# Performance work log

Hardware: AMD Instinct MI355X
Metric: run time of the kernel (lower is better)

The kernel has to match this reference:

```python
import math
import jax, jax.numpy as jnp
import numpy as np

D = 256      # embedding_dim (= internal_dim, downsample_rate 1)
H = 8        # num_heads
HD = D // H  # head_dim = 32
NTC = 16     # num_text_classes
NIMG = 4096  # image tokens (64x64)
N = NIMG + NTC
B = 2
NKE = 64     # num_k_exclude_rope


def _rope(x, freqs):
    # x: (b, h, n, c); freqs: (n, c//2, 2) = (cos, sin) of complex rotary factors
    b, h, n, c = x.shape
    xp = x.reshape(b, h, n, c // 2, 2)
    cos, sin = freqs[..., 0], freqs[..., 1]
    xr, xi = xp[..., 0], xp[..., 1]
    out_r = xr * cos - xi * sin
    out_i = xr * sin + xi * cos
    return jnp.stack([out_r, out_i], axis=-1).reshape(b, h, n, c)


def _sep_heads(x):
    b, n, c = x.shape
    return x.reshape(b, n, H, c // H).transpose(0, 2, 1, 3)  # (b,h,n,hd)


def setup_inputs() -> dict:
    key = jax.random.key(0)
    ks = jax.random.split(key, 14)
    s = 0.02
    # rotary factors: unit-norm cos/sin pairs
    ang_img = jax.random.uniform(ks[3], (NIMG, HD // 2)) * (2.0 * np.pi)
    ang_txt = jax.random.uniform(ks[4], (NTC, HD // 2)) * (2.0 * np.pi)
    return {
        "q": jax.random.normal(ks[0], (B, N, D), dtype=jnp.float32),
        "k": jax.random.normal(ks[1], (B, N, D), dtype=jnp.float32),
        "v": jax.random.normal(ks[2], (B, N, D), dtype=jnp.float32),
        "freqs_cis_img": jnp.stack([jnp.cos(ang_img), jnp.sin(ang_img)], axis=-1),
        "freqs_cis_txt": jnp.stack([jnp.cos(ang_txt), jnp.sin(ang_txt)], axis=-1),
        "Wq": jax.random.normal(ks[5], (D, D), dtype=jnp.float32) * s,
        "bq": jnp.zeros((D,), dtype=jnp.float32),
        "Wk": jax.random.normal(ks[6], (D, D), dtype=jnp.float32) * s,
        "bk": jnp.zeros((D,), dtype=jnp.float32),
        "Wv": jax.random.normal(ks[7], (D, D), dtype=jnp.float32) * s,
        "bv": jnp.zeros((D,), dtype=jnp.float32),
        "Wo": jax.random.normal(ks[8], (D, D), dtype=jnp.float32) * s,
        "bo": jnp.zeros((D,), dtype=jnp.float32),
        "num_k_exclude_rope": NKE,
    }


def reference(q, k, v, freqs_cis_img, freqs_cis_txt,
              Wq, bq, Wk, bk, Wv, bv, Wo, bo, num_k_exclude_rope):
    q = q @ Wq.T + bq
    k = k @ Wk.T + bk
    v = v @ Wv.T + bv
    q = _sep_heads(q)  # (b,h,n,hd)
    k = _sep_heads(k)
    v = _sep_heads(v)

    # split tokens into image / text regions, apply RoPE separately
    q_img, q_txt = q[:, :, :-NTC, :], q[:, :, -NTC:, :]
    k_img, k_txt = k[:, :, :-NTC, :], k[:, :, -NTC:, :]
    q_img = _rope(q_img, freqs_cis_img)
    k_img = _rope(k_img, freqs_cis_img)
    q_txt = _rope(q_txt, freqs_cis_txt)
    k_txt = _rope(k_txt, freqs_cis_txt)
    q = jnp.concatenate([q_img, q_txt], axis=-2)
    k = jnp.concatenate([k_img, k_txt], axis=-2)

    scale = 1.0 / math.sqrt(HD)
    nke = num_k_exclude_rope
    if nke > 0:
        k_td, k_mem = k[:, :, :-nke, :], k[:, :, -nke:, :]
        v_td, v_mem = v[:, :, :-nke, :], v[:, :, -nke:, :]
        attn = jax.nn.softmax(jnp.einsum('bhqd,bhkd->bhqk', q, k_td) * scale, axis=-1)
        out = jnp.einsum('bhqk,bhkd->bhqd', attn, v_td)
        attn_m = jax.nn.softmax(jnp.einsum('bhqd,bhkd->bhqk', q, k_mem) * scale, axis=-1)
        out = out + jnp.einsum('bhqk,bhkd->bhqd', attn_m, v_mem)
    else:
        attn = jax.nn.softmax(jnp.einsum('bhqd,bhkd->bhqk', q, k) * scale, axis=-1)
        out = jnp.einsum('bhqk,bhkd->bhqd', attn, v)

    b, h, n, hd = out.shape
    out = out.transpose(0, 2, 1, 3).reshape(b, n, h * hd)
    return out @ Wo.T + bo
```

## Files before the change

### kernel.cpp

```cpp
#include <hip/hip_runtime.h>
#include <hip/hip_bf16.h>

#define BN    4112
#define NKR   4160
#define BNP   4160
#define BB    2
#define HH    8
#define NIMG_ 4096
#define NMAIN 4048
#define MROWS 8224
#define QSCALE 0.25505402f

typedef __attribute__((ext_vector_type(8))) short short8;
typedef __attribute__((ext_vector_type(4))) float f32x4;
typedef __attribute__((ext_vector_type(16))) float f32x16;

__device__ __forceinline__ unsigned short f2bs(float x) { return __bfloat16_as_ushort(__float2bfloat16(x)); }
__device__ __forceinline__ unsigned pkbf(float a, float b) {
    __hip_bfloat162 h = __float22bfloat162_rn(make_float2(a, b));
    unsigned u; __builtin_memcpy(&u, &h, 4); return u;
}
__device__ __forceinline__ float fexp2(float x) {
#if __has_builtin(__builtin_amdgcn_exp2f)
    return __builtin_amdgcn_exp2f(x);
#else
    return exp2f(x);
#endif
}

__global__ __launch_bounds__(256)
void qkv_mfma(const float* __restrict__ Aq, const float* __restrict__ Ak, const float* __restrict__ Av,
              const float* __restrict__ Wq, const float* __restrict__ Wk, const float* __restrict__ Wv,
              const float* __restrict__ bq, const float* __restrict__ bk, const float* __restrict__ bv,
              short* __restrict__ Qr, short* __restrict__ Kr, short* __restrict__ Vt,
              const float* __restrict__ fimg, const float* __restrict__ ftxt)
{
    __shared__ __align__(16) short Ws[2][64][72];
    __shared__ __align__(16) short Ds[2][64][72];

    const int mode = blockIdx.z;
    const float* A    = (mode == 0) ? Aq : (mode == 1) ? Ak : Av;
    const float* W    = (mode == 0) ? Wq : (mode == 1) ? Wk : Wv;
    const float* bias = (mode == 0) ? bq : (mode == 1) ? bk : bv;

    const int t    = threadIdx.x;
    const int wave = t >> 6, lane = t & 63, q16 = lane & 15, quad = lane >> 4;
    const int f0 = blockIdx.x * 64;
    const int m0 = blockIdx.y * 64;
    const int sr = t >> 2, sc = (t & 3) * 16;
    const int arow = m0 + sr;
    const bool aval = arow < MROWS;
    const float* wp = W + (size_t)(f0 + sr) * 256 + sc;
    const float* ap = A + (size_t)(aval ? arow : 0) * 256 + sc;

    f32x4 acc[4] = {{0,0,0,0},{0,0,0,0},{0,0,0,0},{0,0,0,0}};

    uint4 wr0, wr1, dr0, dr1;
    {
        float4 a0 = *(const float4*)(wp),     a1 = *(const float4*)(wp + 4);
        float4 a2 = *(const float4*)(wp + 8), a3 = *(const float4*)(wp + 12);
        wr0 = uint4{pkbf(a0.x,a0.y), pkbf(a0.z,a0.w), pkbf(a1.x,a1.y), pkbf(a1.z,a1.w)};
        wr1 = uint4{pkbf(a2.x,a2.y), pkbf(a2.z,a2.w), pkbf(a3.x,a3.y), pkbf(a3.z,a3.w)};
        a0 = *(const float4*)(ap);     a1 = *(const float4*)(ap + 4);
        a2 = *(const float4*)(ap + 8); a3 = *(const float4*)(ap + 12);
        dr0 = uint4{pkbf(a0.x,a0.y), pkbf(a0.z,a0.w), pkbf(a1.x,a1.y), pkbf(a1.z,a1.w)};
        dr1 = uint4{pkbf(a2.x,a2.y), pkbf(a2.z,a2.w), pkbf(a3.x,a3.y), pkbf(a3.z,a3.w)};
    }
    *(uint4*)&Ws[0][sr][sc] = wr0; *(uint4*)&Ws[0][sr][sc + 8] = wr1;
    *(uint4*)&Ds[0][sr][sc] = dr0; *(uint4*)&Ds[0][sr][sc + 8] = dr1;
    __syncthreads();

    #pragma unroll
    for (int ki = 0; ki < 4; ++ki) {
        const int buf = ki & 1;
        if (ki < 3) {
            const int k1 = (ki + 1) * 64;
            float4 a0 = *(const float4*)(wp + k1),     a1 = *(const float4*)(wp + k1 + 4);
            float4 a2 = *(const float4*)(wp + k1 + 8), a3 = *(const float4*)(wp + k1 + 12);
            wr0 = uint4{pkbf(a0.x,a0.y), pkbf(a0.z,a0.w), pkbf(a1.x,a1.y), pkbf(a1.z,a1.w)};
            wr1 = uint4{pkbf(a2.x,a2.y), pkbf(a2.z,a2.w), pkbf(a3.x,a3.y), pkbf(a3.z,a3.w)};
            a0 = *(const float4*)(ap + k1);     a1 = *(const float4*)(ap + k1 + 4);
            a2 = *(const float4*)(ap + k1 + 8); a3 = *(const float4*)(ap + k1 + 12);
            dr0 = uint4{pkbf(a0.x,a0.y), pkbf(a0.z,a0.w), pkbf(a1.x,a1.y), pkbf(a1.z,a1.w)};
            dr1 = uint4{pkbf(a2.x,a2.y), pkbf(a2.z,a2.w), pkbf(a3.x,a3.y), pkbf(a3.z,a3.w)};
        }
        #pragma unroll
        for (int ks = 0; ks < 2; ++ks) {
            const short8 af = *(const short8*)&Ws[buf][wave * 16 + q16][ks * 32 + quad * 8];
            #pragma unroll
            for (int ct = 0; ct < 4; ++ct) {
                const short8 bf = *(const short8*)&Ds[buf][ct * 16 + q16][ks * 32 + quad * 8];
                acc[ct] = __builtin_amdgcn_mfma_f32_16x16x32_bf16(af, bf, acc[ct], 0, 0, 0);
            }
        }
        if (ki < 3) {
            *(uint4*)&Ws[buf ^ 1][sr][sc] = wr0; *(uint4*)&Ws[buf ^ 1][sr][sc + 8] = wr1;
            *(uint4*)&Ds[buf ^ 1][sr][sc] = dr0; *(uint4*)&Ds[buf ^ 1][sr][sc + 8] = dr1;
            __syncthreads();
        }
    }

    const int fbase = f0 + wave * 16 + quad * 4;
    const float4 bb = *(const float4*)(bias + fbase);
    float vs[4][4];
    #pragma unroll
    for (int ct = 0; ct < 4; ++ct) {
        int n = m0 + ct * 16 + q16;
        float v0 = acc[ct][0] + bb.x, v1 = acc[ct][1] + bb.y;
        float v2 = acc[ct][2] + bb.z, v3 = acc[ct][3] + bb.w;
        int b  = (n >= BN) ? 1 : 0;
        int nb = n - b * BN;
        if (mode < 2) {
            int j0 = (fbase & 31) >> 1;
            const float* fr = (nb < NIMG_) ? (fimg + ((size_t)nb * 16 + j0) * 2)
                                           : (ftxt + ((size_t)(nb - NIMG_) * 16 + j0) * 2);
            float4 cs = *(const float4*)fr;
            float r0 = v0 * cs.x - v1 * cs.y, i0 = v0 * cs.y + v1 * cs.x;
            float r1 = v2 * cs.z - v3 * cs.w, i1 = v2 * cs.w + v3 * cs.z;
            v0 = r0; v1 = i0; v2 = r1; v3 = i1;
        }
        if (mode == 2) {
            vs[ct][0] = v0; vs[ct][1] = v1; vs[ct][2] = v2; vs[ct][3] = v3;
            continue;
        }
        if (n >= MROWS) continue;
        const int h = (fbase >> 5) & 7, hd = fbase & 31;
        if (mode == 0) {
            unsigned short* op = (unsigned short*)Qr + (((size_t)(b * HH + h) * BN + nb) * 32 + hd);
            *(uint2*)op = uint2{pkbf(v0 * QSCALE, v1 * QSCALE), pkbf(v2 * QSCALE, v3 * QSCALE)};
        } else {
            int nk = nb + ((nb >= NMAIN) ? 48 : 0);
            unsigned short* op = (unsigned short*)Kr + (((size_t)(b * HH + h) * NKR + nk) * 32 + hd);
            *(uint2*)op = uint2{pkbf(v0, v1), pkbf(v2, v3)};
        }
    }

    if (mode == 2) {
        short (*Tr)[72] = Ds[0];
        const int fl = wave * 16 + quad * 4;
        #pragma unroll
        for (int ct = 0; ct < 4; ++ct) {
            const int nl = ct * 16 + q16;
            Tr[fl + 0][nl] = (short)f2bs(vs[ct][0]);
            Tr[fl + 1][nl] = (short)f2bs(vs[ct][1]);
            Tr[fl + 2][nl] = (short)f2bs(vs[ct][2]);
            Tr[fl + 3][nl] = (short)f2bs(vs[ct][3]);
        }
        __syncthreads();
        const int h0 = (f0 >> 5) & 7;
        #pragma unroll
        for (int ii = 0; ii < 2; ++ii) {
            const int r  = ii * 32 + (t >> 3);
            const int c8 = (t & 7) * 8;
            const int ng = m0 + c8;
            if (ng < MROWS) {
                uint4 val = *(const uint4*)&Tr[r][c8];
                int b  = (ng >= BN) ? 1 : 0;
                int nb = ng - b * BN;
                int nk = nb + ((nb >= NMAIN) ? 48 : 0);
                int h  = h0 + (r >> 5), hd = r & 31;
                unsigned short* op = (unsigned short*)Vt + ((size_t)(b * HH + h) * 32 + hd) * BNP + nk;
                *(uint4*)op = val;
            }
        }
    }

    if (blockIdx.x == 0 && blockIdx.y < 16 && t < 192) {
        const int bh = blockIdx.y;
        if (mode == 1) {
            short* base = Kr + (size_t)bh * NKR * 32 + (size_t)NMAIN * 32;
            *(uint4*)(base + t * 8) = uint4{0u, 0u, 0u, 0u};
        } else if (mode == 2) {
            short* base = Vt + (size_t)bh * 32 * BNP + (size_t)(t / 6) * BNP + NMAIN + (t % 6) * 8;
            *(uint4*)base = uint4{0u, 0u, 0u, 0u};
        }
    }
}

__global__ __launch_bounds__(256, 4)
void attn_mfma(const short* __restrict__ Qr, const short* __restrict__ Kr,
               const short* __restrict__ Vt, unsigned short* __restrict__ AO)
{
    __shared__ __align__(16) short Ks[2][2][64][40];
    __shared__ __align__(16) short Vs[2][2][32][72];

    const int t    = threadIdx.x;
    const int wave = t >> 6, lane = t & 63, q32 = lane & 31, hi = lane >> 5;
    const int grp  = wave >> 1, w2 = wave & 1;
    const int bh = blockIdx.y;
    const int q  = blockIdx.x * 64 + w2 * 32 + q32;
    const int qc = (q < BN) ? q : (BN - 1);
    const short* qp = Qr + ((size_t)bh * BN + qc) * 32 + hi * 8;
    const short8 qf0 = *(const short8*)(qp);
    const short8 qf1 = *(const short8*)(qp + 16);

    f32x16 oAx = {0,0,0,0,0,0,0,0,0,0,0,0,0,0,0,0};
    f32x16 oAy = {0,0,0,0,0,0,0,0,0,0,0,0,0,0,0,0};
    f32x16 oBx = {0,0,0,0,0,0,0,0,0,0,0,0,0,0,0,0};
    const f32x16 z16 = {0,0,0,0,0,0,0,0,0,0,0,0,0,0,0,0};
    float LA = 0.f, LB = 0.f;

    const int tg = t & 127;
    const int kr = tg >> 2, kc = tg & 3;
    const int vr = tg >> 3, vc = tg & 7;
    const short* kg = Kr + (size_t)bh * NKR * 32 + (size_t)grp * 65536 + (size_t)kr * 32 + kc * 8;
    const short* vg = Vt + (size_t)bh * 32 * BNP + (size_t)vr * BNP + grp * 2048
                         + (vc >> 1) * 16 + (vc & 1) * 4;
    const int ntiles = 32 + grp;

    auto tile = [&](int buf, f32x16& ox, f32x16& oy, float& L) {
        const short8 kf00 = *(const short8*)&Ks[grp][buf][q32][hi * 8];
        const short8 kf01 = *(const short8*)&Ks[grp][buf][q32][16 + hi * 8];
        const short8 kf10 = *(const short8*)&Ks[grp][buf][32 + q32][hi * 8];
        const short8 kf11 = *(const short8*)&Ks[grp][buf][32 + q32][16 + hi * 8];
        f32x16 s0 = __builtin_amdgcn_mfma_f32_32x32x16_bf16(kf00, qf0, z16, 0, 0, 0);
        f32x16 s1 = __builtin_amdgcn_mfma_f32_32x32x16_bf16(kf10, qf0, z16, 0, 0, 0);
        s0 = __builtin_amdgcn_mfma_f32_32x32x16_bf16(kf01, qf1, s0, 0, 0, 0);
        s1 = __builtin_amdgcn_mfma_f32_32x32x16_bf16(kf11, qf1, s1, 0, 0, 0);
        float p0[16], p1[16];
        #pragma unroll
        for (int r = 0; r < 16; ++r) p0[r] = fexp2(s0[r]);
        #pragma unroll
        for (int r = 0; r < 16; ++r) p1[r] = fexp2(s1[r]);
        float l0 = (((p0[0]+p0[1])+(p0[2]+p0[3])) + ((p0[4]+p0[5])+(p0[6]+p0[7])))
                 + (((p0[8]+p0[9])+(p0[10]+p0[11])) + ((p0[12]+p0[13])+(p0[14]+p0[15])));
        float l1 = (((p1[0]+p1[1])+(p1[2]+p1[3])) + ((p1[4]+p1[5])+(p1[6]+p1[7])))
                 + (((p1[8]+p1[9])+(p1[10]+p1[11])) + ((p1[12]+p1[13])+(p1[14]+p1[15])));
        #pragma unroll
        for (int m = 0; m < 2; ++m) {
            uint4 pbu = uint4{pkbf(p0[8*m+0], p0[8*m+1]), pkbf(p0[8*m+2], p0[8*m+3]),
                              pkbf(p0[8*m+4], p0[8*m+5]), pkbf(p0[8*m+6], p0[8*m+7])};
            short8 pb; __builtin_memcpy(&pb, &pbu, 16);
            const short8 vf = *(const short8*)&Vs[grp][buf][q32][m * 16 + hi * 8];
            ox = __builtin_amdgcn_mfma_f32_32x32x16_bf16(vf, pb, ox, 0, 0, 0);
        }
        #pragma unroll
        for (int m = 0; m < 2; ++m) {
            uint4 pbu = uint4{pkbf(p1[8*m+0], p1[8*m+1]), pkbf(p1[8*m+2], p1[8*m+3]),
                              pkbf(p1[8*m+4], p1[8*m+5]), pkbf(p1[8*m+6], p1[8*m+7])};
            short8 pb; __builtin_memcpy(&pb, &pbu, 16);
            const short8 vf = *(const short8*)&Vs[grp][buf][q32][32 + m * 16 + hi * 8];
            oy = __builtin_amdgcn_mfma_f32_32x32x16_bf16(vf, pb, oy, 0, 0, 0);
        }
        L += l0 + l1;
    };

    *(uint4*)&Ks[grp][0][kr][kc * 8]      = *(const uint4*)(kg);
    *(uint4*)&Ks[grp][0][kr + 32][kc * 8] = *(const uint4*)(kg + 1024);
    {
        uint2 a0 = *(const uint2*)(vg),              b0 = *(const uint2*)(vg + 8);
        uint2 a1 = *(const uint2*)(vg + 16 * BNP),   b1 = *(const uint2*)(vg + 16 * BNP + 8);
        *(uint4*)&Vs[grp][0][vr][vc * 8]      = uint4{a0.x, a0.y, b0.x, b0.y};
        *(uint4*)&Vs[grp][0][vr + 16][vc * 8] = uint4{a1.x, a1.y, b1.x, b1.y};
    }
    __syncthreads();

    for (int it = 0; it < 33; ++it) {
        const int buf = it & 1;
        uint4 kreg0, kreg1; uint2 va0, vb0, va1, vb1;
        const bool pre = (it + 1) < ntiles;
        if (pre) {
            const short* kp = kg + (size_t)(it + 1) * 2048;
            kreg0 = *(const uint4*)(kp);
            kreg1 = *(const uint4*)(kp + 1024);
            const short* vp = vg + (it + 1) * 64;
            va0 = *(const uint2*)(vp);            vb0 = *(const uint2*)(vp + 8);
            va1 = *(const uint2*)(vp + 16 * BNP); vb1 = *(const uint2*)(vp + 16 * BNP + 8);
        }
        if (it < ntiles) {
            __builtin_amdgcn_s_setprio(1);
            if (grp == 0)      tile(buf, oAx, oAy, LA);
            else if (it < 32)  tile(buf, oAx, oAy, LA);
            else               tile(buf, oBx, oBx, LB);
            __builtin_amdgcn_s_setprio(0);
        }
        if (pre) {
            *(uint4*)&Ks[grp][buf ^ 1][kr][kc * 8]      = kreg0;
            *(uint4*)&Ks[grp][buf ^ 1][kr + 32][kc * 8] = kreg1;
            *(uint4*)&Vs[grp][buf ^ 1][vr][vc * 8]      = uint4{va0.x, va0.y, vb0.x, vb0.y};
            *(uint4*)&Vs[grp][buf ^ 1][vr + 16][vc * 8] = uint4{va1.x, va1.y, vb1.x, vb1.y};
        }
        __syncthreads();
    }

    f32x16 oA = oAx + oAy;
    f32x16 oB = oBx;

    LA += __shfl_xor(LA, 32);
    LB += __shfl_xor(LB, 32);

    float* ex = (float*)&Ks[0][0][0][0];
    const int slot = (w2 * 64 + lane) * 20;
    if (grp == 0) {
        #pragma unroll
        for (int i = 0; i < 4; ++i)
            *(f32x4*)(ex + slot + 4 * i) = f32x4{oA[4*i], oA[4*i+1], oA[4*i+2], oA[4*i+3]};
        ex[slot + 16] = LA;
    }
    __syncthreads();

    if (grp == 1 && q < BN) {
        float LT = LA + ex[slot + 16] - 48.f;
        const float iA = 1.f / LT, iB = 1.f / LB;
        const int b = bh >> 3, h = bh & 7;
        unsigned short* ap = AO + ((size_t)b * BN + q) * 256 + h * 32;
        #pragma unroll
        for (int k = 0; k < 4; ++k) {
            f32x4 a = *(const f32x4*)(ex + slot + 4 * k);
            float w0 = (oA[4*k+0] + a[0]) * iA + oB[4*k+0] * iB;
            float w1 = (oA[4*k+1] + a[1]) * iA + oB[4*k+1] * iB;
            float w2 = (oA[4*k+2] + a[2]) * iA + oB[4*k+2] * iB;
            float w3 = (oA[4*k+3] + a[3]) * iA + oB[4*k+3] * iB;
            *(uint2*)(ap + 8 * k + 4 * hi) = uint2{pkbf(w0, w1), pkbf(w2, w3)};
        }
    }
}

__global__ __launch_bounds__(256)
void gemm_out(const unsigned short* __restrict__ A, const float* __restrict__ W,
              const float* __restrict__ bias, float* __restrict__ out)
{
    __shared__ __align__(16) short Ws[2][64][72];
    __shared__ __align__(16) short Ds[2][64][72];
    const int t    = threadIdx.x;
    const int wave = t >> 6, lane = t & 63, q16 = lane & 15, quad = lane >> 4;
    const int f0 = blockIdx.x * 64, m0 = blockIdx.y * 64;
    const int sr = t >> 2, sc = (t & 3) * 16;
    const int arow = m0 + sr;
    const bool aval = arow < MROWS;
    const float* wp = W + (size_t)(f0 + sr) * 256 + sc;
    const unsigned short* ap = A + (size_t)(aval ? arow : 0) * 256 + sc;

    f32x4 acc[4] = {{0,0,0,0},{0,0,0,0},{0,0,0,0},{0,0,0,0}};

    uint4 wr0, wr1, dr0, dr1;
    {
        float4 a0 = *(const float4*)(wp),     a1 = *(const float4*)(wp + 4);
        float4 a2 = *(const float4*)(wp + 8), a3 = *(const float4*)(wp + 12);
        wr0 = uint4{pkbf(a0.x,a0.y), pkbf(a0.z,a0.w), pkbf(a1.x,a1.y), pkbf(a1.z,a1.w)};
        wr1 = uint4{pkbf(a2.x,a2.y), pkbf(a2.z,a2.w), pkbf(a3.x,a3.y), pkbf(a3.z,a3.w)};
        dr0 = *(const uint4*)(ap); dr1 = *(const uint4*)(ap + 8);
    }
    *(uint4*)&Ws[0][sr][sc] = wr0; *(uint4*)&Ws[0][sr][sc + 8] = wr1;
    *(uint4*)&Ds[0][sr][sc] = dr0; *(uint4*)&Ds[0][sr][sc + 8] = dr1;
    __syncthreads();

    #pragma unroll
    for (int ki = 0; ki < 4; ++ki) {
        const int buf = ki & 1;
        if (ki < 3) {
            const int k1 = (ki + 1) * 64;
            float4 a0 = *(const float4*)(wp + k1),     a1 = *(const float4*)(wp + k1 + 4);
            float4 a2 = *(const float4*)(wp + k1 + 8), a3 = *(const float4*)(wp + k1 + 12);
            wr0 = uint4{pkbf(a0.x,a0.y), pkbf(a0.z,a0.w), pkbf(a1.x,a1.y), pkbf(a1.z,a1.w)};
            wr1 = uint4{pkbf(a2.x,a2.y), pkbf(a2.z,a2.w), pkbf(a3.x,a3.y), pkbf(a3.z,a3.w)};
            dr0 = *(const uint4*)(ap + k1); dr1 = *(const uint4*)(ap + k1 + 8);
        }
        #pragma unroll
        for (int ks = 0; ks < 2; ++ks) {
            const short8 af = *(const short8*)&Ws[buf][wave * 16 + q16][ks * 32 + quad * 8];
            #pragma unroll
            for (int ct = 0; ct < 4; ++ct) {
                const short8 bf = *(const short8*)&Ds[buf][ct * 16 + q16][ks * 32 + quad * 8];
                acc[ct] = __builtin_amdgcn_mfma_f32_16x16x32_bf16(af, bf, acc[ct], 0, 0, 0);
            }
        }
        if (ki < 3) {
            *(uint4*)&Ws[buf ^ 1][sr][sc] = wr0; *(uint4*)&Ws[buf ^ 1][sr][sc + 8] = wr1;
            *(uint4*)&Ds[buf ^ 1][sr][sc] = dr0; *(uint4*)&Ds[buf ^ 1][sr][sc + 8] = dr1;
            __syncthreads();
        }
    }

    const int fbase = f0 + wave * 16 + quad * 4;
    const float4 bb = *(const float4*)(bias + fbase);
    #pragma unroll
    for (int ct = 0; ct < 4; ++ct) {
        int n = m0 + ct * 16 + q16;
        if (n >= MROWS) continue;
        float* op = out + (size_t)n * 256 + fbase;
        *(float4*)op = float4{acc[ct][0] + bb.x, acc[ct][1] + bb.y,
                              acc[ct][2] + bb.z, acc[ct][3] + bb.w};
    }
}

extern "C" void kernel_launch(void* const* d_in, const int* in_sizes, int n_in,
                              void* d_out, int out_size, void* d_ws, size_t ws_size,
                              hipStream_t stream)
{
    (void)in_sizes; (void)n_in; (void)out_size; (void)ws_size;
    const float* q    = (const float*)d_in[0];
    const float* k    = (const float*)d_in[1];
    const float* v    = (const float*)d_in[2];
    const float* fimg = (const float*)d_in[3];
    const float* ftxt = (const float*)d_in[4];
    const float* Wq   = (const float*)d_in[5];
    const float* bq   = (const float*)d_in[6];
    const float* Wk   = (const float*)d_in[7];
    const float* bk   = (const float*)d_in[8];
    const float* Wv   = (const float*)d_in[9];
    const float* bv   = (const float*)d_in[10];
    const float* Wo   = (const float*)d_in[11];
    const float* bo   = (const float*)d_in[12];

    char* w = (char*)d_ws;
    short*          Qr = (short*)(w);
    short*          Kr = (short*)(w + 4210688);
    short*          Vt = (short*)(w + 8470528);
    unsigned short* AO = (unsigned short*)(w + 12730368);

    qkv_mfma<<<dim3(4, 129, 3), 256, 0, stream>>>(q, k, v, Wq, Wk, Wv, bq, bk, bv,
                                                  Qr, Kr, Vt, fimg, ftxt);
    attn_mfma<<<dim3(65, 16), 256, 0, stream>>>(Qr, Kr, Vt, AO);
    gemm_out<<<dim3(4, 129), 256, 0, stream>>>(AO, Wo, bo, (float*)d_out);
}
```

Before: 202.2 us.

## Prefetch K/V two tiles ahead and remap attention grid for XCD locality

The attention loop now issues global K/V loads two tiles ahead, using two register staging sets, and is unrolled by two so loads overlap more MFMA/exp work. The grid is flattened to 1D with an index remap that round-robins heads across consecutive block IDs, so each head's K/V blocks share an L2/XCD. The extra staging registers may raise register pressure and lower occupancy.

```diff
diff --git a/kernel.cpp b/kernel.cpp
--- a/kernel.cpp
+++ b/kernel.cpp
@@ -187,8 +187,13 @@
     const int t    = threadIdx.x;
     const int wave = t >> 6, lane = t & 63, q32 = lane & 31, hi = lane >> 5;
     const int grp  = wave >> 1, w2 = wave & 1;
-    const int bh = blockIdx.y;
-    const int q  = blockIdx.x * 64 + w2 * 32 + q32;
+
+    const int b_   = blockIdx.x;
+    const int idx  = b_ >> 3;
+    const int bh   = ((b_ & 7) << 1) + (idx >= 65 ? 1 : 0);
+    const int bx   = idx - (idx >= 65 ? 65 : 0);
+
+    const int q  = bx * 64 + w2 * 32 + q32;
     const int qc = (q < BN) ? q : (BN - 1);
     const short* qp = Qr + ((size_t)bh * BN + qc) * 32 + hi * 8;
     const short8 qf0 = *(const short8*)(qp);
@@ -207,6 +212,22 @@
     const short* vg = Vt + (size_t)bh * 32 * BNP + (size_t)vr * BNP + grp * 2048
                          + (vc >> 1) * 16 + (vc & 1) * 4;
     const int ntiles = 32 + grp;
+
+    struct Stage { uint4 k0, k1; uint2 a0, b0, a1, b1; };
+    auto issue = [&](int tix, Stage& s) {
+        const short* kp = kg + (size_t)tix * 2048;
+        s.k0 = *(const uint4*)(kp);
+        s.k1 = *(const uint4*)(kp + 1024);
+        const short* vp = vg + tix * 64;
+        s.a0 = *(const uint2*)(vp);            s.b0 = *(const uint2*)(vp + 8);
+        s.a1 = *(const uint2*)(vp + 16 * BNP); s.b1 = *(const uint2*)(vp + 16 * BNP + 8);
+    };
+    auto commit = [&](int buf, const Stage& s) {
+        *(uint4*)&Ks[grp][buf][kr][kc * 8]      = s.k0;
+        *(uint4*)&Ks[grp][buf][kr + 32][kc * 8] = s.k1;
+        *(uint4*)&Vs[grp][buf][vr][vc * 8]      = uint4{s.a0.x, s.a0.y, s.b0.x, s.b0.y};
+        *(uint4*)&Vs[grp][buf][vr + 16][vc * 8] = uint4{s.a1.x, s.a1.y, s.b1.x, s.b1.y};
+    };
 
     auto tile = [&](int buf, f32x16& ox, f32x16& oy, float& L) {
         const short8 kf00 = *(const short8*)&Ks[grp][buf][q32][hi * 8];
@@ -245,42 +266,38 @@
         L += l0 + l1;
     };
 
-    *(uint4*)&Ks[grp][0][kr][kc * 8]      = *(const uint4*)(kg);
-    *(uint4*)&Ks[grp][0][kr + 32][kc * 8] = *(const uint4*)(kg + 1024);
+    Stage sA, sB;
     {
-        uint2 a0 = *(const uint2*)(vg),              b0 = *(const uint2*)(vg + 8);
-        uint2 a1 = *(const uint2*)(vg + 16 * BNP),   b1 = *(const uint2*)(vg + 16 * BNP + 8);
-        *(uint4*)&Vs[grp][0][vr][vc * 8]      = uint4{a0.x, a0.y, b0.x, b0.y};
-        *(uint4*)&Vs[grp][0][vr + 16][vc * 8] = uint4{a1.x, a1.y, b1.x, b1.y};
-    }
+        Stage s0s; issue(0, s0s); commit(0, s0s);
+    }
+    issue(1, sB);
     __syncthreads();
 
-    for (int it = 0; it < 33; ++it) {
-        const int buf = it & 1;
-        uint4 kreg0, kreg1; uint2 va0, vb0, va1, vb1;
-        const bool pre = (it + 1) < ntiles;
-        if (pre) {
-            const short* kp = kg + (size_t)(it + 1) * 2048;
-            kreg0 = *(const uint4*)(kp);
-            kreg1 = *(const uint4*)(kp + 1024);
-            const short* vp = vg + (it + 1) * 64;
-            va0 = *(const uint2*)(vp);            vb0 = *(const uint2*)(vp + 8);
-            va1 = *(const uint2*)(vp + 16 * BNP); vb1 = *(const uint2*)(vp + 16 * BNP + 8);
-        }
-        if (it < ntiles) {
-            __builtin_amdgcn_s_setprio(1);
-            if (grp == 0)      tile(buf, oAx, oAy, LA);
-            else if (it < 32)  tile(buf, oAx, oAy, LA);
-            else               tile(buf, oBx, oBx, LB);
-            __builtin_amdgcn_s_setprio(0);
-        }
-        if (pre) {
-            *(uint4*)&Ks[grp][buf ^ 1][kr][kc * 8]      = kreg0;
-            *(uint4*)&Ks[grp][buf ^ 1][kr + 32][kc * 8] = kreg1;
-            *(uint4*)&Vs[grp][buf ^ 1][vr][vc * 8]      = uint4{va0.x, va0.y, vb0.x, vb0.y};
-            *(uint4*)&Vs[grp][buf ^ 1][vr + 16][vc * 8] = uint4{va1.x, va1.y, vb1.x, vb1.y};
-        }
-        __syncthreads();
+    for (int itb = 0; itb < 34; itb += 2) {
+        {
+            const int it = itb;
+            if (it + 2 < ntiles) issue(it + 2, sA);
+            if (it < ntiles) {
+                __builtin_amdgcn_s_setprio(1);
+                if (grp == 0 || it < 32) tile(it & 1, oAx, oAy, LA);
+                else                     tile(it & 1, oBx, oBx, LB);
+                __builtin_amdgcn_s_setprio(0);
+            }
+            if (it + 1 < ntiles) commit((it + 1) & 1, sB);
+            __syncthreads();
+        }
+        {
+            const int it = itb + 1;
+            if (it + 2 < ntiles) issue(it + 2, sB);
+            if (it < ntiles) {
+                __builtin_amdgcn_s_setprio(1);
+                if (grp == 0 || it < 32) tile(it & 1, oAx, oAy, LA);
+                else                     tile(it & 1, oBx, oBx, LB);
+                __builtin_amdgcn_s_setprio(0);
+            }
+            if (it + 1 < ntiles) commit((it + 1) & 1, sA);
+            __syncthreads();
+        }
     }
 
     f32x16 oA = oAx + oAy;
@@ -411,6 +428,6 @@
 
     qkv_mfma<<<dim3(4, 129, 3), 256, 0, stream>>>(q, k, v, Wq, Wk, Wv, bq, bk, bv,
                                                   Qr, Kr, Vt, fimg, ftxt);
-    attn_mfma<<<dim3(65, 16), 256, 0, stream>>>(Qr, Kr, Vt, AO);
+    attn_mfma<<<dim3(1040), 256, 0, stream>>>(Qr, Kr, Vt, AO);
     gemm_out<<<dim3(4, 129), 256, 0, stream>>>(AO, Wo, bo, (float*)d_out);
 }
```

Result: slower. 361.4 us (+78.8%).
